# Performance work log

Measured on AMD Instinct MI355X. Metric: run time of the kernel, lower is better.

The kernel has to match this reference:

```python
import jax, jax.numpy as jnp
import numpy as np

N = 100000
E = 3200000
D = 128
H = 128
BN_EPS = 1e-5


def setup_inputs() -> dict:
    key = jax.random.key(0)
    ks = jax.random.split(key, 8)
    x = jax.random.normal(ks[0], (N, D), dtype=jnp.float32)
    edge_index = jax.random.randint(ks[1], (2, E), 0, N, dtype=jnp.int64)
    edge_attr = jax.random.normal(ks[2], (E, 1), dtype=jnp.float32)
    # MLP params (Linear stores weight [out,in]; we keep [in,out] for x @ W)
    W1 = jax.random.normal(ks[3], (D, H), dtype=jnp.float32) / np.sqrt(D)
    b1 = jnp.zeros((H,), dtype=jnp.float32)
    W2 = jax.random.normal(ks[4], (H, H), dtype=jnp.float32) / np.sqrt(H)
    b2 = jnp.zeros((H,), dtype=jnp.float32)
    gamma = jnp.ones((H,), dtype=jnp.float32)
    beta = jnp.zeros((H,), dtype=jnp.float32)
    return {"x": x, "edge_index": edge_index, "edge_attr": edge_attr,
            "W1": W1, "b1": b1, "W2": W2, "b2": b2,
            "gamma": gamma, "beta": beta}


def reference(x, edge_index, edge_attr, W1, b1, W2, b2, gamma, beta):
    src, dst = edge_index[0], edge_index[1]
    # GIN aggregation: (1 + eps) * x_i + sum_{j->i} x_j, eps = 0
    agg = jax.ops.segment_sum(x[src], dst, num_segments=N)  # [N, D]
    h = x + agg
    # 2-layer MLP
    h = jax.nn.relu(h @ W1 + b1)
    h = h @ W2 + b2
    # outer ReLU
    h = jax.nn.relu(h)
    # BatchNorm1d (training mode: batch stats, biased variance)
    mean = jnp.mean(h, axis=0)
    var = jnp.mean(jnp.square(h - mean), axis=0)
    h = (h - mean) * jax.lax.rsqrt(var + BN_EPS) * gamma + beta
    return h
```

## Files before the change

### kernel.cpp

```cpp
#include <hip/hip_runtime.h>

#define N_NODES 100000
#define DIM 128
#define NBUCK 391
#define CAP 12288
#define PT_TILE 8192
#define PT_THR 512

typedef unsigned int u32;
typedef unsigned short u16;
typedef __attribute__((ext_vector_type(8))) short bf16x8;
typedef __attribute__((ext_vector_type(4))) float f32x4;

__device__ __forceinline__ float bf16_to_f(u16 v) {
  return __uint_as_float(((u32)v) << 16);
}
__device__ __forceinline__ u16 f_to_bf16(float f) {
  u32 b = __float_as_uint(f);
  b += 0x7fff + ((b >> 16) & 1);
  return (u16)(b >> 16);
}
__device__ __forceinline__ float blo(u32 q) { return __uint_as_float(q << 16); }
__device__ __forceinline__ float bhi(u32 q) {
  return __uint_as_float(q & 0xffff0000u);
}

__global__ __launch_bounds__(256) void prep_kernel(
    const float* __restrict__ x, u16* __restrict__ xb,
    const float* __restrict__ W1, u16* __restrict__ Wt1,
    const float* __restrict__ W2, u16* __restrict__ Wt2,
    int* __restrict__ bcnt, float* __restrict__ stats) {
  int blk = blockIdx.x;
  if (blk < 2048) {
    int total = N_NODES * DIM / 4;
    int stride = 2048 * 256;
    for (int i = blk * 256 + threadIdx.x; i < total; i += stride) {
      float4 v = reinterpret_cast<const float4*>(x)[i];
      ushort4 o;
      o.x = f_to_bf16(v.x);
      o.y = f_to_bf16(v.y);
      o.z = f_to_bf16(v.z);
      o.w = f_to_bf16(v.w);
      reinterpret_cast<ushort4*>(xb)[i] = o;
    }
  } else if (blk < 2112) {
    int id = (blk - 2048) * 256 + threadIdx.x;
    Wt1[id] = f_to_bf16(W1[(id & 127) * DIM + (id >> 7)]);
  } else if (blk < 2176) {
    int id = (blk - 2112) * 256 + threadIdx.x;
    Wt2[id] = f_to_bf16(W2[(id & 127) * DIM + (id >> 7)]);
  } else {
    int t = threadIdx.x;
    for (int i = t; i < 400; i += 256) bcnt[i] = 0;
    for (int i = t; i < 768; i += 256) stats[i] = 0.f;
  }
}

__global__ __launch_bounds__(256) void bhist_kernel(const int* __restrict__ ei,
                                                    int* __restrict__ bcnt,
                                                    int E_) {
  __shared__ int lc[NBUCK];
  for (int i = threadIdx.x; i < NBUCK; i += 256) lc[i] = 0;
  __syncthreads();
  const int* dst = ei + E_;
  int G = gridDim.x * blockDim.x;
  int g = blockIdx.x * blockDim.x + threadIdx.x;
  int n4 = E_ >> 2;
  const int4* d4 = (const int4*)dst;
  for (int i = g; i < n4; i += G) {
    int4 v = d4[i];
    atomicAdd(&lc[((u32)v.x) >> 8], 1);
    atomicAdd(&lc[((u32)v.y) >> 8], 1);
    atomicAdd(&lc[((u32)v.z) >> 8], 1);
    atomicAdd(&lc[((u32)v.w) >> 8], 1);
  }
  for (int e = (n4 << 2) + g; e < E_; e += G)
    atomicAdd(&lc[((u32)dst[e]) >> 8], 1);
  __syncthreads();
  for (int i = threadIdx.x; i < NBUCK; i += 256)
    if (lc[i]) atomicAdd(&bcnt[i], lc[i]);
}

__global__ void bscan_kernel(const int* __restrict__ bcnt,
                             int* __restrict__ boffs, int* __restrict__ gcur) {
  __shared__ int s[256];
  int t = threadIdx.x;
  int v0 = (2 * t < NBUCK) ? bcnt[2 * t] : 0;
  int v1 = (2 * t + 1 < NBUCK) ? bcnt[2 * t + 1] : 0;
  int ts = v0 + v1;
  s[t] = ts;
  __syncthreads();
  for (int o = 1; o < 256; o <<= 1) {
    int u = (t >= o) ? s[t - o] : 0;
    __syncthreads();
    s[t] += u;
    __syncthreads();
  }
  int excl = s[t] - ts;
  if (2 * t <= NBUCK) boffs[2 * t] = excl;
  if (2 * t + 1 <= NBUCK) boffs[2 * t + 1] = excl + v0;
  if (2 * t < NBUCK) gcur[2 * t] = excl;
  if (2 * t + 1 < NBUCK) gcur[2 * t + 1] = excl + v0;
}

__global__ __launch_bounds__(PT_THR) void partition_kernel(
    const int* __restrict__ ei, int* __restrict__ gcur,
    u32* __restrict__ packed, int E_) {
  __shared__ u32 keys[PT_TILE];
  __shared__ u16 bid[PT_TILE];
  __shared__ int lh[NBUCK];
  __shared__ int lpos[NBUCK];
  __shared__ int gpos[NBUCK];
  __shared__ int ss[PT_THR];
  const int t = threadIdx.x;
  const int base = blockIdx.x * PT_TILE;
  const int cnt = min(PT_TILE, E_ - base);

  for (int i = t; i < NBUCK; i += PT_THR) lh[i] = 0;
  __syncthreads();

  u32 pk[16];
  int bb[16];
#pragma unroll
  for (int k = 0; k < 16; ++k) {
    int e = base + k * PT_THR + t;
    if (k * PT_THR + t < cnt) {
      int src = ei[e];
      u32 dst = (u32)ei[E_ + e];
      bb[k] = (int)(dst >> 8);
      pk[k] = (u32)src | ((dst & 255u) << 17);
      atomicAdd(&lh[bb[k]], 1);
    } else {
      bb[k] = -1;
    }
  }
  __syncthreads();

  int v = (t < NBUCK) ? lh[t] : 0;
  ss[t] = v;
  __syncthreads();
  for (int o = 1; o < PT_THR; o <<= 1) {
    int u = (t >= o) ? ss[t - o] : 0;
    __syncthreads();
    ss[t] += u;
    __syncthreads();
  }
  if (t < NBUCK) {
    lpos[t] = ss[t] - v;
    if (v > 0) gpos[t] = atomicAdd(&gcur[t], v);
  }
  __syncthreads();

#pragma unroll
  for (int k = 0; k < 16; ++k) {
    if (bb[k] >= 0) {
      int p = atomicAdd(&lpos[bb[k]], 1);
      keys[p] = pk[k];
      bid[p] = (u16)bb[k];
    }
  }
  __syncthreads();

  for (int i = t; i < cnt; i += PT_THR) {
    int b = bid[i];
    int startb = lpos[b] - lh[b];
    packed[gpos[b] + (i - startb)] = keys[i];
  }
}

__global__ __launch_bounds__(256) void bsort_kernel(u32* __restrict__ packed,
                                                    const int* __restrict__ boffs,
                                                    int* __restrict__ offs,
                                                    int E_) {
  __shared__ u32 sorted_[CAP];
  __shared__ int hist[256], cur[256], ss[256];
  const int b = blockIdx.x, t = threadIdx.x;
  int base = boffs[b];
  int cnt = boffs[b + 1] - base;
  if (cnt > CAP) cnt = CAP;
  hist[t] = 0;
  __syncthreads();
  for (int i = t; i < cnt; i += 256) atomicAdd(&hist[packed[base + i] >> 17], 1);
  __syncthreads();
  int hv = hist[t];
  ss[t] = hv;
  __syncthreads();
  for (int o = 1; o < 256; o <<= 1) {
    int u = (t >= o) ? ss[t - o] : 0;
    __syncthreads();
    ss[t] += u;
    __syncthreads();
  }
  int excl = ss[t] - hv;
  cur[t] = excl;
  __syncthreads();
  for (int i = t; i < cnt; i += 256) {
    u32 v = packed[base + i];
    int p = atomicAdd(&cur[v >> 17], 1);
    sorted_[p] = v & 0x1FFFFu;
  }
  __syncthreads();
  for (int i = t; i < cnt; i += 256) packed[base + i] = sorted_[i];
  int node = b * 256 + t;
  if (node < N_NODES) offs[node] = base + excl;
  if (b == 0 && t == 0) offs[N_NODES] = E_;
}

__global__ __launch_bounds__(256) void gather_bf16_kernel(
    const u32* __restrict__ xb, const int* __restrict__ offs,
    const int* __restrict__ csr, u32* __restrict__ hb) {
  int n = blockIdx.x * 4 + (threadIdx.x >> 6);
  int lane = threadIdx.x & 63;
  int beg = offs[n], end = offs[n + 1];
  u32 p = xb[(size_t)n * 64 + lane];
  float a0 = blo(p), a1 = bhi(p);
  float b0 = 0.f, b1 = 0.f, c0 = 0.f, c1 = 0.f, d0 = 0.f, d1 = 0.f;
  int j = beg;
  while (j < end && (j & 3)) {
    u32 q = xb[(size_t)csr[j] * 64 + lane];
    a0 += blo(q);
    a1 += bhi(q);
    ++j;
  }
  for (; j + 16 <= end; j += 16) {
    int4 i0 = *reinterpret_cast<const int4*>(csr + j);
    int4 i1 = *reinterpret_cast<const int4*>(csr + j + 4);
    int4 i2 = *reinterpret_cast<const int4*>(csr + j + 8);
    int4 i3 = *reinterpret_cast<const int4*>(csr + j + 12);
    u32 q0 = xb[(size_t)i0.x * 64 + lane];
    u32 q1 = xb[(size_t)i0.y * 64 + lane];
    u32 q2 = xb[(size_t)i0.z * 64 + lane];
    u32 q3 = xb[(size_t)i0.w * 64 + lane];
    u32 q4 = xb[(size_t)i1.x * 64 + lane];
    u32 q5 = xb[(size_t)i1.y * 64 + lane];
    u32 q6 = xb[(size_t)i1.z * 64 + lane];
    u32 q7 = xb[(size_t)i1.w * 64 + lane];
    u32 q8 = xb[(size_t)i2.x * 64 + lane];
    u32 q9 = xb[(size_t)i2.y * 64 + lane];
    u32 qa = xb[(size_t)i2.z * 64 + lane];
    u32 qb = xb[(size_t)i2.w * 64 + lane];
    u32 qc = xb[(size_t)i3.x * 64 + lane];
    u32 qd = xb[(size_t)i3.y * 64 + lane];
    u32 qe = xb[(size_t)i3.z * 64 + lane];
    u32 qf = xb[(size_t)i3.w * 64 + lane];
    a0 += blo(q0); a1 += bhi(q0);
    b0 += blo(q1); b1 += bhi(q1);
    c0 += blo(q2); c1 += bhi(q2);
    d0 += blo(q3); d1 += bhi(q3);
    a0 += blo(q4); a1 += bhi(q4);
    b0 += blo(q5); b1 += bhi(q5);
    c0 += blo(q6); c1 += bhi(q6);
    d0 += blo(q7); d1 += bhi(q7);
    a0 += blo(q8); a1 += bhi(q8);
    b0 += blo(q9); b1 += bhi(q9);
    c0 += blo(qa); c1 += bhi(qa);
    d0 += blo(qb); d1 += bhi(qb);
    a0 += blo(qc); a1 += bhi(qc);
    b0 += blo(qd); b1 += bhi(qd);
    c0 += blo(qe); c1 += bhi(qe);
    d0 += blo(qf); d1 += bhi(qf);
  }
  for (; j + 4 <= end; j += 4) {
    int4 i0 = *reinterpret_cast<const int4*>(csr + j);
    u32 q0 = xb[(size_t)i0.x * 64 + lane];
    u32 q1 = xb[(size_t)i0.y * 64 + lane];
    u32 q2 = xb[(size_t)i0.z * 64 + lane];
    u32 q3 = xb[(size_t)i0.w * 64 + lane];
    a0 += blo(q0); a1 += bhi(q0);
    b0 += blo(q1); b1 += bhi(q1);
    c0 += blo(q2); c1 += bhi(q2);
    d0 += blo(q3); d1 += bhi(q3);
  }
  for (; j < end; ++j) {
    u32 q = xb[(size_t)csr[j] * 64 + lane];
    a0 += blo(q);
    a1 += bhi(q);
  }
  a0 += b0 + c0 + d0;
  a1 += b1 + c1 + d1;
  hb[(size_t)n * 64 + lane] = ((u32)f_to_bf16(a1) << 16) | (u32)f_to_bf16(a0);
}

__global__ __launch_bounds__(256) void mlp_mfma_kernel(
    const u16* __restrict__ hb, const u16* __restrict__ Wt1,
    const u16* __restrict__ Wt2, const float* __restrict__ b1,
    const float* __restrict__ b2, float* __restrict__ out,
    float* __restrict__ pstats) {
  __shared__ u16 sH1[4][16 * DIM];
  __shared__ float sS[4][128], sQ[4][128];
  const int tid = threadIdx.x;
  const int wv = tid >> 6;
  const int lane = tid & 63;
  const int lr = lane & 15;
  const int lq = lane >> 4;
  const int row0 = blockIdx.x * 64 + wv * 16;

  bf16x8 a[4];
  {
    int r = row0 + lr;
    if (r > N_NODES - 1) r = N_NODES - 1;
#pragma unroll
    for (int ks = 0; ks < 4; ++ks)
      a[ks] = *reinterpret_cast<const bf16x8*>(hb + (size_t)r * DIM + ks * 32 +
                                               lq * 8);
  }
  f32x4 acc[8];
#pragma unroll
  for (int ct = 0; ct < 8; ++ct) {
    f32x4 c = {0.f, 0.f, 0.f, 0.f};
#pragma unroll
    for (int ks = 0; ks < 4; ++ks) {
      bf16x8 b = *reinterpret_cast<const bf16x8*>(
          Wt1 + (ct * 16 + lr) * DIM + ks * 32 + lq * 8);
      c = __builtin_amdgcn_mfma_f32_16x16x32_bf16(a[ks], b, c, 0, 0, 0);
    }
    acc[ct] = c;
  }
  char* slab = reinterpret_cast<char*>(&sH1[wv][0]);
#pragma unroll
  for (int ct = 0; ct < 8; ++ct) {
    int c = ct * 16 + lr;
    float bias = b1[c];
#pragma unroll
    for (int j = 0; j < 4; ++j) {
      int rl = lq * 4 + j;
      float y = fmaxf(acc[ct][j] + bias, 0.f);
      int byte = rl * 256 + ((c * 2) ^ ((rl & 7) << 4));
      *reinterpret_cast<u16*>(slab + byte) = f_to_bf16(y);
    }
  }
  __syncthreads();

  bf16x8 a2[4];
#pragma unroll
  for (int ks = 0; ks < 4; ++ks) {
    int byte = lr * 256 + (((ks * 32 + lq * 8) * 2) ^ ((lr & 7) << 4));
    a2[ks] = *reinterpret_cast<const bf16x8*>(slab + byte);
  }
#pragma unroll
  for (int ct = 0; ct < 8; ++ct) {
    f32x4 c = {0.f, 0.f, 0.f, 0.f};
#pragma unroll
    for (int ks = 0; ks < 4; ++ks) {
      bf16x8 b = *reinterpret_cast<const bf16x8*>(
          Wt2 + (ct * 16 + lr) * DIM + ks * 32 + lq * 8);
      c = __builtin_amdgcn_mfma_f32_16x16x32_bf16(a2[ks], b, c, 0, 0, 0);
    }
    acc[ct] = c;
  }
  float ls[8], lss[8];
#pragma unroll
  for (int ct = 0; ct < 8; ++ct) {
    int c = ct * 16 + lr;
    float bias = b2[c];
    ls[ct] = 0.f;
    lss[ct] = 0.f;
#pragma unroll
    for (int j = 0; j < 4; ++j) {
      int r = row0 + lq * 4 + j;
      float y = fmaxf(acc[ct][j] + bias, 0.f);
      if (r < N_NODES) {
        out[(size_t)r * DIM + c] = y;
        ls[ct] += y;
        lss[ct] += y * y;
      }
    }
  }
#pragma unroll
  for (int ct = 0; ct < 8; ++ct) {
    float s = ls[ct], q = lss[ct];
    s += __shfl_xor(s, 16);
    q += __shfl_xor(q, 16);
    s += __shfl_xor(s, 32);
    q += __shfl_xor(q, 32);
    if (lq == 0) {
      sS[wv][ct * 16 + lr] = s;
      sQ[wv][ct * 16 + lr] = q;
    }
  }
  __syncthreads();
  {
    int t = tid;
    float v;
    if (t < 128)
      v = sS[0][t] + sS[1][t] + sS[2][t] + sS[3][t];
    else
      v = sQ[0][t - 128] + sQ[1][t - 128] + sQ[2][t - 128] + sQ[3][t - 128];
    pstats[(size_t)blockIdx.x * 256 + t] = v;
  }
}

__global__ __launch_bounds__(256) void bn_reduce_kernel(
    const float* __restrict__ pstats, float* __restrict__ stats, int nblk) {
  int t = threadIdx.x;
  float v = 0.f;
  for (int i = blockIdx.x; i < nblk; i += gridDim.x)
    v += pstats[(size_t)i * 256 + t];
  atomicAdd(&stats[t], v);
}

__global__ void bn_scale_kernel(const float* __restrict__ stats,
                                const float* __restrict__ gamma,
                                const float* __restrict__ beta,
                                float* __restrict__ sc) {
  int c = threadIdx.x;
  float mean = stats[c] / (float)N_NODES;
  float var = stats[DIM + c] / (float)N_NODES - mean * mean;
  float scale = gamma[c] * rsqrtf(var + 1e-5f);
  sc[c] = scale;
  sc[DIM + c] = beta[c] - mean * scale;
}

__global__ __launch_bounds__(256) void bn_apply_kernel(
    float* __restrict__ h, const float* __restrict__ sc) {
  size_t total = (size_t)N_NODES * DIM / 4;
  size_t stride = (size_t)gridDim.x * blockDim.x;
  for (size_t i = (size_t)blockIdx.x * blockDim.x + threadIdx.x; i < total;
       i += stride) {
    float4 v = reinterpret_cast<float4*>(h)[i];
    int c = (int)((i * 4) & 127);
    v.x = v.x * sc[c + 0] + sc[DIM + c + 0];
    v.y = v.y * sc[c + 1] + sc[DIM + c + 1];
    v.z = v.z * sc[c + 2] + sc[DIM + c + 2];
    v.w = v.w * sc[c + 3] + sc[DIM + c + 3];
    reinterpret_cast<float4*>(h)[i] = v;
  }
}

__global__ __launch_bounds__(256) void hist_kernel(const int* __restrict__ ei,
                                                   int* __restrict__ deg,
                                                   int E_) {
  int stride = gridDim.x * blockDim.x;
  for (int e = blockIdx.x * blockDim.x + threadIdx.x; e < E_; e += stride)
    atomicAdd(&deg[ei[E_ + e]], 1);
}

__global__ __launch_bounds__(256) void scan_block_kernel(
    const int* __restrict__ deg, int* __restrict__ offs,
    int* __restrict__ partials, int n) {
  const int tid = threadIdx.x;
  int g = blockIdx.x * 1024 + tid * 4;
  int v0 = (g + 0 < n) ? deg[g + 0] : 0;
  int v1 = (g + 1 < n) ? deg[g + 1] : 0;
  int v2 = (g + 2 < n) ? deg[g + 2] : 0;
  int v3 = (g + 3 < n) ? deg[g + 3] : 0;
  int tsum = v0 + v1 + v2 + v3;
  __shared__ int s[256];
  s[tid] = tsum;
  __syncthreads();
  for (int off = 1; off < 256; off <<= 1) {
    int t = (tid >= off) ? s[tid - off] : 0;
    __syncthreads();
    s[tid] += t;
    __syncthreads();
  }
  int excl = s[tid] - tsum;
  if (g + 0 < n) offs[g + 0] = excl;
  if (g + 1 < n) offs[g + 1] = excl + v0;
  if (g + 2 < n) offs[g + 2] = excl + v0 + v1;
  if (g + 3 < n) offs[g + 3] = excl + v0 + v1 + v2;
  if (tid == 255) partials[blockIdx.x] = s[255];
}

__global__ void scan_partials_kernel(int* __restrict__ partials, int nb) {
  const int tid = threadIdx.x;
  int v = (tid < nb) ? partials[tid] : 0;
  __shared__ int s[128];
  s[tid] = v;
  __syncthreads();
  for (int off = 1; off < 128; off <<= 1) {
    int t = (tid >= off) ? s[tid - off] : 0;
    __syncthreads();
    s[tid] += t;
    __syncthreads();
  }
  if (tid < nb) partials[tid] = s[tid] - v;
}

__global__ __launch_bounds__(256) void scan_add_kernel(
    int* __restrict__ offs, int* __restrict__ cursor,
    const int* __restrict__ partials, int n, int E_) {
  int g = blockIdx.x * blockDim.x + threadIdx.x;
  if (g < n) {
    int v = offs[g] + partials[g >> 10];
    offs[g] = v;
    cursor[g] = v;
  }
  if (g == 0) offs[n] = E_;
}

__global__ __launch_bounds__(256) void fill_kernel(const int* __restrict__ ei,
                                                   int* __restrict__ cursor,
                                                   int* __restrict__ csr,
                                                   int E_) {
  const int G = gridDim.x * blockDim.x;
  int g = blockIdx.x * blockDim.x + threadIdx.x;
  for (long long base = g; base < E_; base += (long long)G * 8) {
    int src[8], dst[8], pos[8];
#pragma unroll
    for (int k = 0; k < 8; ++k) {
      long long e = base + (long long)k * G;
      src[k] = (e < E_) ? ei[e] : -1;
      dst[k] = (e < E_) ? ei[E_ + e] : 0;
    }
#pragma unroll
    for (int k = 0; k < 8; ++k)
      if (src[k] >= 0) pos[k] = atomicAdd(&cursor[dst[k]], 1);
#pragma unroll
    for (int k = 0; k < 8; ++k)
      if (src[k] >= 0) csr[pos[k]] = src[k];
  }
}

__global__ __launch_bounds__(128) void gather_f32_kernel(
    const float* __restrict__ x, const int* __restrict__ offs,
    const int* __restrict__ csr, float* __restrict__ h) {
  int n = blockIdx.x;
  int c = threadIdx.x;
  int beg = offs[n], end = offs[n + 1];
  float acc = x[(size_t)n * DIM + c];
  for (int j = beg; j < end; ++j) acc += x[(size_t)csr[j] * DIM + c];
  h[(size_t)n * DIM + c] = acc;
}

__global__ __launch_bounds__(256) void scatter_kernel(
    const float* __restrict__ x, const int* __restrict__ ei,
    float* __restrict__ h, int E_) {
  long long total = (long long)E_ * 32;
  long long stride = (long long)gridDim.x * blockDim.x;
  for (long long idx = (long long)blockIdx.x * blockDim.x + threadIdx.x;
       idx < total; idx += stride) {
    int e = (int)(idx >> 5);
    int q = (int)(idx & 31);
    float4 v =
        *reinterpret_cast<const float4*>(x + (size_t)ei[e] * DIM + q * 4);
    float* p = h + (size_t)ei[E_ + e] * DIM + q * 4;
    atomicAdd(p + 0, v.x);
    atomicAdd(p + 1, v.y);
    atomicAdd(p + 2, v.z);
    atomicAdd(p + 3, v.w);
  }
}

__global__ __launch_bounds__(256) void add_x_kernel(const float* __restrict__ x,
                                                    float* __restrict__ h) {
  size_t total = (size_t)N_NODES * DIM / 4;
  size_t stride = (size_t)gridDim.x * blockDim.x;
  for (size_t i = (size_t)blockIdx.x * blockDim.x + threadIdx.x; i < total;
       i += stride) {
    float4 v = reinterpret_cast<float4*>(h)[i];
    float4 xv = reinterpret_cast<const float4*>(x)[i];
    v.x += xv.x; v.y += xv.y; v.z += xv.z; v.w += xv.w;
    reinterpret_cast<float4*>(h)[i] = v;
  }
}

__global__ __launch_bounds__(256) void mlp_valu_kernel(
    float* hbuf, const float* __restrict__ W1, const float* __restrict__ b1,
    const float* __restrict__ W2, const float* __restrict__ b2) {
  __shared__ float sW[DIM * DIM];
  __shared__ float sH[32][DIM];
  const int tid = threadIdx.x;
  const int col = tid & 127;
  const int rhalf = tid >> 7;
  const int row0 = blockIdx.x * 32;

  for (int i = tid; i < DIM * DIM; i += 256) sW[i] = W1[i];
  for (int i = tid; i < 32 * DIM; i += 256) {
    int r = i >> 7, c = i & 127;
    sH[r][c] = hbuf[(size_t)(row0 + r) * DIM + c];
  }
  __syncthreads();
  float acc[16];
  float bias = b1[col];
#pragma unroll
  for (int j = 0; j < 16; ++j) acc[j] = bias;
#pragma unroll 4
  for (int k = 0; k < DIM; ++k) {
    float w = sW[k * DIM + col];
#pragma unroll
    for (int j = 0; j < 16; ++j) acc[j] = fmaf(sH[2 * j + rhalf][k], w, acc[j]);
  }
  __syncthreads();
  for (int i = tid; i < DIM * DIM; i += 256) sW[i] = W2[i];
#pragma unroll
  for (int j = 0; j < 16; ++j) sH[2 * j + rhalf][col] = fmaxf(acc[j], 0.f);
  __syncthreads();
  float bias2 = b2[col];
#pragma unroll
  for (int j = 0; j < 16; ++j) acc[j] = bias2;
#pragma unroll 4
  for (int k = 0; k < DIM; ++k) {
    float w = sW[k * DIM + col];
#pragma unroll
    for (int j = 0; j < 16; ++j) acc[j] = fmaf(sH[2 * j + rhalf][k], w, acc[j]);
  }
#pragma unroll
  for (int j = 0; j < 16; ++j)
    hbuf[(size_t)(row0 + 2 * j + rhalf) * DIM + col] = fmaxf(acc[j], 0.f);
}

__global__ __launch_bounds__(256) void bn_stats_kernel(
    const float* __restrict__ h, float* __restrict__ stats) {
  int col = threadIdx.x & 127;
  int rsub = threadIdx.x >> 7;
  int rstep = gridDim.x * 2;
  float s = 0.f, ss = 0.f;
  for (int r = blockIdx.x * 2 + rsub; r < N_NODES; r += rstep) {
    float v = h[(size_t)r * DIM + col];
    s += v;
    ss += v * v;
  }
  __shared__ float ls[256], lss[256];
  ls[threadIdx.x] = s;
  lss[threadIdx.x] = ss;
  __syncthreads();
  if (threadIdx.x < 128) {
    atomicAdd(&stats[col], ls[threadIdx.x] + ls[threadIdx.x + 128]);
    atomicAdd(&stats[DIM + col], lss[threadIdx.x] + lss[threadIdx.x + 128]);
  }
}

extern "C" void kernel_launch(void* const* d_in, const int* in_sizes, int n_in,
                              void* d_out, int out_size, void* d_ws,
                              size_t ws_size, hipStream_t stream) {
  const float* x = (const float*)d_in[0];
  const int* ei = (const int*)d_in[1];
  const float* W1 = (const float*)d_in[3];
  const float* b1 = (const float*)d_in[4];
  const float* W2 = (const float*)d_in[5];
  const float* b2 = (const float*)d_in[6];
  const float* gamma = (const float*)d_in[7];
  const float* beta = (const float*)d_in[8];
  float* out = (float*)d_out;
  int E_ = in_sizes[1] / 2;

  const size_t XB_B = (size_t)N_NODES * DIM * 2;
  char* w = (char*)d_ws;
  size_t off = 0;
  u16* xb = (u16*)(w + off); off += XB_B;
  u16* hb = (u16*)(w + off); off += XB_B;
  u16* Wt1 = (u16*)(w + off); off += 32768;
  u16* Wt2 = (u16*)(w + off); off += 32768;
  u32* packed = (u32*)(w + off); off += (size_t)E_ * 4;
  int* offs = (int*)(w + off); off += ((size_t)N_NODES + 4) * 4;
  int* bcnt = (int*)(w + off); off += 1600;
  float* stats = (float*)(w + off); off += 3072;
  int* boffs = (int*)(w + off); off += 1600;
  int* gcur = (int*)(w + off); off += 1600;
  size_t need_full = off;
  float* pstats = (float*)xb;

  int* f_offs = (int*)d_ws;
  int* f_cursor = f_offs + N_NODES + 1;
  int* f_partials = f_cursor + N_NODES;
  int* f_csr = f_partials + 128;
  float* f_stats = (float*)(f_csr + E_);
  size_t need_csr = ((size_t)2 * N_NODES + 129 + E_) * 4 + 3072;

  const int nScanBlocks = (N_NODES + 1023) / 1024;
  const int nEdgeBlocks = (E_ + 2047) / 2048;
  const int nPartBlocks = (E_ + PT_TILE - 1) / PT_TILE;
  const int nMlpBlocks = (N_NODES + 63) / 64;

  if (ws_size >= need_full) {
    prep_kernel<<<2177, 256, 0, stream>>>(x, xb, W1, Wt1, W2, Wt2, bcnt,
                                          stats);
    bhist_kernel<<<512, 256, 0, stream>>>(ei, bcnt, E_);
    bscan_kernel<<<1, 256, 0, stream>>>(bcnt, boffs, gcur);
    partition_kernel<<<nPartBlocks, PT_THR, 0, stream>>>(ei, gcur, packed, E_);
    bsort_kernel<<<NBUCK, 256, 0, stream>>>(packed, boffs, offs, E_);
    gather_bf16_kernel<<<N_NODES / 4, 256, 0, stream>>>((const u32*)xb, offs,
                                                        (const int*)packed,
                                                        (u32*)hb);
    mlp_mfma_kernel<<<nMlpBlocks, 256, 0, stream>>>(hb, Wt1, Wt2, b1, b2, out,
                                                    pstats);
    bn_reduce_kernel<<<32, 256, 0, stream>>>(pstats, stats, nMlpBlocks);
    bn_scale_kernel<<<1, 128, 0, stream>>>(stats, gamma, beta, stats + 256);
    bn_apply_kernel<<<2048, 256, 0, stream>>>(out, stats + 256);
  } else if (ws_size >= need_csr) {
    hipMemsetAsync(f_cursor, 0, (size_t)N_NODES * sizeof(int), stream);
    hipMemsetAsync(f_stats, 0, 768 * sizeof(float), stream);
    hist_kernel<<<2048, 256, 0, stream>>>(ei, f_cursor, E_);
    scan_block_kernel<<<nScanBlocks, 256, 0, stream>>>(f_cursor, f_offs,
                                                       f_partials, N_NODES);
    scan_partials_kernel<<<1, 128, 0, stream>>>(f_partials, nScanBlocks);
    scan_add_kernel<<<(N_NODES + 255) / 256, 256, 0, stream>>>(
        f_offs, f_cursor, f_partials, N_NODES, E_);
    fill_kernel<<<nEdgeBlocks, 256, 0, stream>>>(ei, f_cursor, f_csr, E_);
    gather_f32_kernel<<<N_NODES, 128, 0, stream>>>(x, f_offs, f_csr, out);
    mlp_valu_kernel<<<(N_NODES + 31) / 32, 256, 0, stream>>>(out, W1, b1, W2,
                                                             b2);
    bn_stats_kernel<<<1024, 256, 0, stream>>>(out, f_stats);
    bn_scale_kernel<<<1, 128, 0, stream>>>(f_stats, gamma, beta, f_stats + 256);
    bn_apply_kernel<<<2048, 256, 0, stream>>>(out, f_stats + 256);
  } else {
    float* s2 = (float*)d_ws;
    hipMemsetAsync(out, 0, (size_t)N_NODES * DIM * sizeof(float), stream);
    hipMemsetAsync(s2, 0, 768 * sizeof(float), stream);
    scatter_kernel<<<4096, 256, 0, stream>>>(x, ei, out, E_);
    add_x_kernel<<<2048, 256, 0, stream>>>(x, out);
    mlp_valu_kernel<<<(N_NODES + 31) / 32, 256, 0, stream>>>(out, W1, b1, W2,
                                                             b2);
    bn_stats_kernel<<<1024, 256, 0, stream>>>(out, s2);
    bn_scale_kernel<<<1, 128, 0, stream>>>(s2, gamma, beta, s2 + 256);
    bn_apply_kernel<<<2048, 256, 0, stream>>>(out, s2 + 256);
  }
}
```

Before: 286.5 us.

## Vectorize gather to 16-byte loads across four edge groups; fuse histogram into prep

The gather kernel now has each wave split into four 16-lane groups. Each group loads a full 256-byte bf16 row with 16-byte uint4 loads and handles every fourth edge, and partial sums are combined with cross-lane shuffles. This replaces 4-byte-per-lane loads with wider loads and more edges in flight per wave. The bucket histogram is merged into the prep kernel as extra blocks, and counter zeroing moves to a memset, which removes one launch. The risks are extra shuffle work, strided csr index reads, and that the memset now zeroes stats and bcnt together, which assumes they are contiguous in the workspace.

```diff
diff --git a/kernel.cpp b/kernel.cpp
--- a/kernel.cpp
+++ b/kernel.cpp
@@ -24,12 +24,15 @@
 __device__ __forceinline__ float bhi(u32 q) {
   return __uint_as_float(q & 0xffff0000u);
 }
+__device__ __forceinline__ u32 packbf(float lo, float hi) {
+  return ((u32)f_to_bf16(hi) << 16) | (u32)f_to_bf16(lo);
+}
 
 __global__ __launch_bounds__(256) void prep_kernel(
     const float* __restrict__ x, u16* __restrict__ xb,
     const float* __restrict__ W1, u16* __restrict__ Wt1,
     const float* __restrict__ W2, u16* __restrict__ Wt2,
-    int* __restrict__ bcnt, float* __restrict__ stats) {
+    const int* __restrict__ ei, int* __restrict__ bcnt, int E_) {
   int blk = blockIdx.x;
   if (blk < 2048) {
     int total = N_NODES * DIM / 4;
@@ -50,35 +53,27 @@
     int id = (blk - 2112) * 256 + threadIdx.x;
     Wt2[id] = f_to_bf16(W2[(id & 127) * DIM + (id >> 7)]);
   } else {
-    int t = threadIdx.x;
-    for (int i = t; i < 400; i += 256) bcnt[i] = 0;
-    for (int i = t; i < 768; i += 256) stats[i] = 0.f;
-  }
-}
-
-__global__ __launch_bounds__(256) void bhist_kernel(const int* __restrict__ ei,
-                                                    int* __restrict__ bcnt,
-                                                    int E_) {
-  __shared__ int lc[NBUCK];
-  for (int i = threadIdx.x; i < NBUCK; i += 256) lc[i] = 0;
-  __syncthreads();
-  const int* dst = ei + E_;
-  int G = gridDim.x * blockDim.x;
-  int g = blockIdx.x * blockDim.x + threadIdx.x;
-  int n4 = E_ >> 2;
-  const int4* d4 = (const int4*)dst;
-  for (int i = g; i < n4; i += G) {
-    int4 v = d4[i];
-    atomicAdd(&lc[((u32)v.x) >> 8], 1);
-    atomicAdd(&lc[((u32)v.y) >> 8], 1);
-    atomicAdd(&lc[((u32)v.z) >> 8], 1);
-    atomicAdd(&lc[((u32)v.w) >> 8], 1);
-  }
-  for (int e = (n4 << 2) + g; e < E_; e += G)
-    atomicAdd(&lc[((u32)dst[e]) >> 8], 1);
-  __syncthreads();
-  for (int i = threadIdx.x; i < NBUCK; i += 256)
-    if (lc[i]) atomicAdd(&bcnt[i], lc[i]);
+    __shared__ int lc[NBUCK];
+    for (int i = threadIdx.x; i < NBUCK; i += 256) lc[i] = 0;
+    __syncthreads();
+    const int* dst = ei + E_;
+    int G = 512 * 256;
+    int g = (blk - 2176) * 256 + threadIdx.x;
+    int n4 = E_ >> 2;
+    const int4* d4 = (const int4*)dst;
+    for (int i = g; i < n4; i += G) {
+      int4 v = d4[i];
+      atomicAdd(&lc[((u32)v.x) >> 8], 1);
+      atomicAdd(&lc[((u32)v.y) >> 8], 1);
+      atomicAdd(&lc[((u32)v.z) >> 8], 1);
+      atomicAdd(&lc[((u32)v.w) >> 8], 1);
+    }
+    for (int e = (n4 << 2) + g; e < E_; e += G)
+      atomicAdd(&lc[((u32)dst[e]) >> 8], 1);
+    __syncthreads();
+    for (int i = threadIdx.x; i < NBUCK; i += 256)
+      if (lc[i]) atomicAdd(&bcnt[i], lc[i]);
+  }
 }
 
 __global__ void bscan_kernel(const int* __restrict__ bcnt,
@@ -207,78 +202,69 @@
 }
 
 __global__ __launch_bounds__(256) void gather_bf16_kernel(
-    const u32* __restrict__ xb, const int* __restrict__ offs,
-    const int* __restrict__ csr, u32* __restrict__ hb) {
+    const uint4* __restrict__ xb4, const int* __restrict__ offs,
+    const int* __restrict__ csr, uint4* __restrict__ hb4) {
   int n = blockIdx.x * 4 + (threadIdx.x >> 6);
   int lane = threadIdx.x & 63;
+  int g = lane >> 4;
+  int l = lane & 15;
   int beg = offs[n], end = offs[n + 1];
-  u32 p = xb[(size_t)n * 64 + lane];
-  float a0 = blo(p), a1 = bhi(p);
-  float b0 = 0.f, b1 = 0.f, c0 = 0.f, c1 = 0.f, d0 = 0.f, d1 = 0.f;
-  int j = beg;
-  while (j < end && (j & 3)) {
-    u32 q = xb[(size_t)csr[j] * 64 + lane];
-    a0 += blo(q);
-    a1 += bhi(q);
-    ++j;
-  }
-  for (; j + 16 <= end; j += 16) {
-    int4 i0 = *reinterpret_cast<const int4*>(csr + j);
-    int4 i1 = *reinterpret_cast<const int4*>(csr + j + 4);
-    int4 i2 = *reinterpret_cast<const int4*>(csr + j + 8);
-    int4 i3 = *reinterpret_cast<const int4*>(csr + j + 12);
-    u32 q0 = xb[(size_t)i0.x * 64 + lane];
-    u32 q1 = xb[(size_t)i0.y * 64 + lane];
-    u32 q2 = xb[(size_t)i0.z * 64 + lane];
-    u32 q3 = xb[(size_t)i0.w * 64 + lane];
-    u32 q4 = xb[(size_t)i1.x * 64 + lane];
-    u32 q5 = xb[(size_t)i1.y * 64 + lane];
-    u32 q6 = xb[(size_t)i1.z * 64 + lane];
-    u32 q7 = xb[(size_t)i1.w * 64 + lane];
-    u32 q8 = xb[(size_t)i2.x * 64 + lane];
-    u32 q9 = xb[(size_t)i2.y * 64 + lane];
-    u32 qa = xb[(size_t)i2.z * 64 + lane];
-    u32 qb = xb[(size_t)i2.w * 64 + lane];
-    u32 qc = xb[(size_t)i3.x * 64 + lane];
-    u32 qd = xb[(size_t)i3.y * 64 + lane];
-    u32 qe = xb[(size_t)i3.z * 64 + lane];
-    u32 qf = xb[(size_t)i3.w * 64 + lane];
-    a0 += blo(q0); a1 += bhi(q0);
-    b0 += blo(q1); b1 += bhi(q1);
-    c0 += blo(q2); c1 += bhi(q2);
-    d0 += blo(q3); d1 += bhi(q3);
-    a0 += blo(q4); a1 += bhi(q4);
-    b0 += blo(q5); b1 += bhi(q5);
-    c0 += blo(q6); c1 += bhi(q6);
-    d0 += blo(q7); d1 += bhi(q7);
-    a0 += blo(q8); a1 += bhi(q8);
-    b0 += blo(q9); b1 += bhi(q9);
-    c0 += blo(qa); c1 += bhi(qa);
-    d0 += blo(qb); d1 += bhi(qb);
-    a0 += blo(qc); a1 += bhi(qc);
-    b0 += blo(qd); b1 += bhi(qd);
-    c0 += blo(qe); c1 += bhi(qe);
-    d0 += blo(qf); d1 += bhi(qf);
-  }
-  for (; j + 4 <= end; j += 4) {
-    int4 i0 = *reinterpret_cast<const int4*>(csr + j);
-    u32 q0 = xb[(size_t)i0.x * 64 + lane];
-    u32 q1 = xb[(size_t)i0.y * 64 + lane];
-    u32 q2 = xb[(size_t)i0.z * 64 + lane];
-    u32 q3 = xb[(size_t)i0.w * 64 + lane];
-    a0 += blo(q0); a1 += bhi(q0);
-    b0 += blo(q1); b1 += bhi(q1);
-    c0 += blo(q2); c1 += bhi(q2);
-    d0 += blo(q3); d1 += bhi(q3);
-  }
-  for (; j < end; ++j) {
-    u32 q = xb[(size_t)csr[j] * 64 + lane];
-    a0 += blo(q);
-    a1 += bhi(q);
-  }
-  a0 += b0 + c0 + d0;
-  a1 += b1 + c1 + d1;
-  hb[(size_t)n * 64 + lane] = ((u32)f_to_bf16(a1) << 16) | (u32)f_to_bf16(a0);
+  float a0 = 0.f, a1 = 0.f, a2 = 0.f, a3 = 0.f;
+  float a4 = 0.f, a5 = 0.f, a6 = 0.f, a7 = 0.f;
+  if (g == 0) {
+    uint4 q = xb4[(size_t)n * 16 + l];
+    a0 = blo(q.x); a1 = bhi(q.x);
+    a2 = blo(q.y); a3 = bhi(q.y);
+    a4 = blo(q.z); a5 = bhi(q.z);
+    a6 = blo(q.w); a7 = bhi(q.w);
+  }
+  int j = beg + g;
+  for (; j + 12 < end; j += 16) {
+    int s0 = csr[j], s1 = csr[j + 4], s2 = csr[j + 8], s3 = csr[j + 12];
+    uint4 q0 = xb4[(size_t)s0 * 16 + l];
+    uint4 q1 = xb4[(size_t)s1 * 16 + l];
+    uint4 q2 = xb4[(size_t)s2 * 16 + l];
+    uint4 q3 = xb4[(size_t)s3 * 16 + l];
+    a0 += blo(q0.x); a1 += bhi(q0.x);
+    a2 += blo(q0.y); a3 += bhi(q0.y);
+    a4 += blo(q0.z); a5 += bhi(q0.z);
+    a6 += blo(q0.w); a7 += bhi(q0.w);
+    a0 += blo(q1.x); a1 += bhi(q1.x);
+    a2 += blo(q1.y); a3 += bhi(q1.y);
+    a4 += blo(q1.z); a5 += bhi(q1.z);
+    a6 += blo(q1.w); a7 += bhi(q1.w);
+    a0 += blo(q2.x); a1 += bhi(q2.x);
+    a2 += blo(q2.y); a3 += bhi(q2.y);
+    a4 += blo(q2.z); a5 += bhi(q2.z);
+    a6 += blo(q2.w); a7 += bhi(q2.w);
+    a0 += blo(q3.x); a1 += bhi(q3.x);
+    a2 += blo(q3.y); a3 += bhi(q3.y);
+    a4 += blo(q3.z); a5 += bhi(q3.z);
+    a6 += blo(q3.w); a7 += bhi(q3.w);
+  }
+  for (; j < end; j += 4) {
+    uint4 q = xb4[(size_t)csr[j] * 16 + l];
+    a0 += blo(q.x); a1 += bhi(q.x);
+    a2 += blo(q.y); a3 += bhi(q.y);
+    a4 += blo(q.z); a5 += bhi(q.z);
+    a6 += blo(q.w); a7 += bhi(q.w);
+  }
+  a0 += __shfl_xor(a0, 16); a1 += __shfl_xor(a1, 16);
+  a2 += __shfl_xor(a2, 16); a3 += __shfl_xor(a3, 16);
+  a4 += __shfl_xor(a4, 16); a5 += __shfl_xor(a5, 16);
+  a6 += __shfl_xor(a6, 16); a7 += __shfl_xor(a7, 16);
+  a0 += __shfl_xor(a0, 32); a1 += __shfl_xor(a1, 32);
+  a2 += __shfl_xor(a2, 32); a3 += __shfl_xor(a3, 32);
+  a4 += __shfl_xor(a4, 32); a5 += __shfl_xor(a5, 32);
+  a6 += __shfl_xor(a6, 32); a7 += __shfl_xor(a7, 32);
+  if (g == 0) {
+    uint4 o;
+    o.x = packbf(a0, a1);
+    o.y = packbf(a2, a3);
+    o.z = packbf(a4, a5);
+    o.w = packbf(a6, a7);
+    hb4[(size_t)n * 16 + l] = o;
+  }
 }
 
 __global__ __launch_bounds__(256) void mlp_mfma_kernel(
@@ -664,15 +650,14 @@
   const int nMlpBlocks = (N_NODES + 63) / 64;
 
   if (ws_size >= need_full) {
-    prep_kernel<<<2177, 256, 0, stream>>>(x, xb, W1, Wt1, W2, Wt2, bcnt,
-                                          stats);
-    bhist_kernel<<<512, 256, 0, stream>>>(ei, bcnt, E_);
+    hipMemsetAsync(bcnt, 0, 1600 + 3072, stream);
+    prep_kernel<<<2688, 256, 0, stream>>>(x, xb, W1, Wt1, W2, Wt2, ei, bcnt,
+                                          E_);
     bscan_kernel<<<1, 256, 0, stream>>>(bcnt, boffs, gcur);
     partition_kernel<<<nPartBlocks, PT_THR, 0, stream>>>(ei, gcur, packed, E_);
     bsort_kernel<<<NBUCK, 256, 0, stream>>>(packed, boffs, offs, E_);
-    gather_bf16_kernel<<<N_NODES / 4, 256, 0, stream>>>((const u32*)xb, offs,
-                                                        (const int*)packed,
-                                                        (u32*)hb);
+    gather_bf16_kernel<<<N_NODES / 4, 256, 0, stream>>>(
+        (const uint4*)xb, offs, (const int*)packed, (uint4*)hb);
     mlp_mfma_kernel<<<nMlpBlocks, 256, 0, stream>>>(hb, Wt1, Wt2, b1, b2, out,
                                                     pstats);
     bn_reduce_kernel<<<32, 256, 0, stream>>>(pstats, stats, nMlpBlocks);
```

New measurement: 284.6 us. Within noise of the previous version (-0.7%).
